# Kernel tuning notes

Hardware: AMD Instinct MI355X
Metric: run time of the kernel (lower is better)

## Reference

```python
import jax, jax.numpy as jnp
import numpy as np

NUM_EMBEDDINGS = 512
EMBEDDING_DIM = 64
COMMITMENT_COST = 0.25


def setup_inputs() -> dict:
    key = jax.random.key(0)
    k1, k2 = jax.random.split(key)
    inputs = jax.random.normal(k1, (32, EMBEDDING_DIM, 64, 64), dtype=jnp.float32)
    # nn.Embedding weight init: uniform(-1/K, 1/K)
    weight = jax.random.uniform(
        k2, (NUM_EMBEDDINGS, EMBEDDING_DIM), dtype=jnp.float32,
        minval=-1.0 / NUM_EMBEDDINGS, maxval=1.0 / NUM_EMBEDDINGS)
    return {"inputs": inputs, "weight": weight}


def reference(inputs, weight):
    # NCHW -> NHWC
    x = jnp.transpose(inputs, (0, 2, 3, 1))
    B, H, W, D = x.shape
    flat = x.reshape(-1, D)  # [N, D]
    # squared L2 distances to each code: [N, K]
    distances = (jnp.sum(flat * flat, axis=1, keepdims=True)
                 - 2.0 * flat @ weight.T
                 + jnp.sum(weight * weight, axis=1))
    idx = jnp.argmin(distances, axis=1)  # [N]
    # one-hot @ weight == gather (one-hot entries are exactly 0/1)
    quantized = jnp.take(weight, idx, axis=0).reshape(B, H, W, D)
    e_latent_loss = jnp.mean((jax.lax.stop_gradient(quantized) - x) ** 2)
    q_latent_loss = jnp.mean((quantized - jax.lax.stop_gradient(x)) ** 2)
    loss = q_latent_loss + COMMITMENT_COST * e_latent_loss
    # straight-through estimator
    quantized_st = x + jax.lax.stop_gradient(quantized - x)
    discrete_latent = idx.reshape(B, H, W)
    quantized_out = jnp.transpose(quantized_st, (0, 3, 1, 2))  # NHWC -> NCHW
    return discrete_latent, quantized_out, loss
```

## Files before the change

kernel.cpp:

```cpp
#include <hip/hip_runtime.h>

typedef unsigned long long ull;

#define NUM_K   512
#define DIM     64
#define N_ROWS  (32 * 64 * 64)
#define HW      4096
#define CHW     (64 * 4096)

#define IDX_OFF  0
#define Q_OFF    N_ROWS
#define LOSS_OFF (N_ROWS + 32 * 64 * 4096)

#define CAP     8
#define TILE_R4 128
#define NBLK4   (N_ROWS / TILE_R4)
#define NEPI    1024

#define WK1S    1.0e-4f
#define WK2S    2.0e-5f

#define WS_FRAG_LO   16384
#define WS_W2_OFF    32768
#define WS_SWMAX_OFF 33792
#define WS_LSL_BYTE  147456
#define WS_NEED      (147456 + NEPI * 8)

typedef __attribute__((ext_vector_type(8))) short bf16x8;
typedef __attribute__((ext_vector_type(4))) float f32x4;

typedef unsigned uGLB __attribute__((address_space(1)));
typedef unsigned uLDS __attribute__((address_space(3)));
#define GLD16(g, l) __builtin_amdgcn_global_load_lds((const uGLB*)(g), (uLDS*)(l), 16, 0, 0)

#define NP_SUMSQ64(SRC, DST)                                                   \
    do {                                                                       \
        float r_[8];                                                           \
        _Pragma("unroll")                                                      \
        for (int j_ = 0; j_ < 8; ++j_) r_[j_] = __fmul_rn((SRC)[j_], (SRC)[j_]); \
        _Pragma("unroll")                                                      \
        for (int i_ = 8; i_ < 64; i_ += 8) {                                   \
            _Pragma("unroll")                                                  \
            for (int j_ = 0; j_ < 8; ++j_)                                     \
                r_[j_] = __fadd_rn(r_[j_], __fmul_rn((SRC)[i_ + j_], (SRC)[i_ + j_])); \
        }                                                                      \
        (DST) = __fadd_rn(__fadd_rn(__fadd_rn(r_[0], r_[1]), __fadd_rn(r_[2], r_[3])), \
                          __fadd_rn(__fadd_rn(r_[4], r_[5]), __fadd_rn(r_[6], r_[7]))); \
    } while (0)

#define NP_SUMSQ64_G(XC, DST)                                                  \
    do {                                                                       \
        float r_[8];                                                           \
        _Pragma("unroll")                                                      \
        for (int j_ = 0; j_ < 8; ++j_) {                                       \
            float v_ = (XC)[(size_t)j_ * HW];                                  \
            r_[j_] = __fmul_rn(v_, v_);                                        \
        }                                                                      \
        _Pragma("unroll")                                                      \
        for (int i_ = 8; i_ < 64; i_ += 8) {                                   \
            _Pragma("unroll")                                                  \
            for (int j_ = 0; j_ < 8; ++j_) {                                   \
                float v_ = (XC)[(size_t)(i_ + j_) * HW];                       \
                r_[j_] = __fadd_rn(r_[j_], __fmul_rn(v_, v_));                 \
            }                                                                  \
        }                                                                      \
        (DST) = __fadd_rn(__fadd_rn(__fadd_rn(r_[0], r_[1]), __fadd_rn(r_[2], r_[3])), \
                          __fadd_rn(__fadd_rn(r_[4], r_[5]), __fadd_rn(r_[6], r_[7]))); \
    } while (0)

__device__ __forceinline__ unsigned bf16rn(float f) {
    unsigned u = __float_as_uint(f);
    return (u + 0x7fffu + ((u >> 16) & 1u)) >> 16;
}
__device__ __forceinline__ float bf2f(unsigned h) { return __uint_as_float(h << 16); }
__device__ __forceinline__ unsigned pk2(float lo, float hi) {
    return bf16rn(lo) | (bf16rn(hi) << 16);
}

__device__ __forceinline__ float evald(const float* __restrict__ xr,
                                       const float* __restrict__ wc,
                                       float A, float w2c) {
    float m = 0.0f;
    #pragma unroll
    for (int d = 0; d < DIM; ++d) m = __fmaf_rn(xr[d], wc[d], m);
    return __fadd_rn(__fsub_rn(A, __fmul_rn(2.0f, m)), w2c);
}
__device__ __forceinline__ float evald_g(const float* __restrict__ xcol,
                                         const float* __restrict__ wc,
                                         float A, float w2c) {
    float m = 0.0f;
    #pragma unroll
    for (int d = 0; d < DIM; ++d) m = __fmaf_rn(xcol[(size_t)d * HW], wc[d], m);
    return __fadd_rn(__fsub_rn(A, __fmul_rn(2.0f, m)), w2c);
}

__global__ __launch_bounds__(64) void vq_prep(const float* __restrict__ weight,
                                              unsigned* __restrict__ ws) {
    const int c = blockIdx.x * 64 + threadIdx.x;
    const float* wr = weight + c * DIM;
    float wv[DIM];
    #pragma unroll
    for (int d = 0; d < DIM; d += 4) {
        float4 t4 = *(const float4*)&wr[d];
        wv[d] = t4.x; wv[d + 1] = t4.y; wv[d + 2] = t4.z; wv[d + 3] = t4.w;
    }
    float s; NP_SUMSQ64(wv, s);
    ((float*)(ws + WS_W2_OFF))[c] = s;
    float sa = 0.0f;
    #pragma unroll
    for (int d = 0; d < DIM; ++d) sa = __fadd_rn(sa, fabsf(wv[d]));
    float sv = sa * 1.0002f + 1e-7f;

    const int tb = (c >> 4) * 512;
    const int ls = (c & 15) * 4;
    #pragma unroll
    for (int g = 0; g < 8; ++g) {
        int base = tb + (g >> 2) * 256 + (g & 3) * 64 + ls;
        unsigned hu[4], lu[4];
        #pragma unroll
        for (int p = 0; p < 4; ++p) {
            float e0 = wv[8 * g + 2 * p], e1 = wv[8 * g + 2 * p + 1];
            unsigned h0 = bf16rn(e0), h1 = bf16rn(e1);
            float r0 = __fsub_rn(e0, bf2f(h0));
            float r1 = __fsub_rn(e1, bf2f(h1));
            hu[p] = h0 | (h1 << 16);
            lu[p] = bf16rn(r0) | (bf16rn(r1) << 16);
        }
        *(uint4*)&ws[base] = make_uint4(hu[0], hu[1], hu[2], hu[3]);
        *(uint4*)&ws[WS_FRAG_LO + base] = make_uint4(lu[0], lu[1], lu[2], lu[3]);
    }
    #pragma unroll
    for (int mk = 1; mk <= 32; mk <<= 1) sv = fmaxf(sv, __shfl_xor(sv, mk));
    if (threadIdx.x == 0) ((float*)(ws + WS_SWMAX_OFF))[blockIdx.x] = sv;
}

__global__ __launch_bounds__(256, 3) void vq_mfma6(const float* __restrict__ x_in,
                                                   const float* __restrict__ weight,
                                                   const unsigned* __restrict__ frg,
                                                   const float* __restrict__ w2g,
                                                   float* __restrict__ out) {
    __shared__ __align__(16) unsigned dbuf[2][4096];
    __shared__ int   cntL[TILE_R4];
    __shared__ unsigned short listL[TILE_R4 * CAP];

    const int tid   = threadIdx.x;
    const int lane  = tid & 63;
    const int wid   = tid >> 6;
    const int wbase = wid * 32;
    const int qid   = lane >> 4;
    const int l15   = lane & 15;

    const int rowbase = blockIdx.x * TILE_R4;
    const int b       = rowbase >> 12;
    const int hw0     = rowbase & 4095;
    const float* xb   = x_in + (size_t)b * CHW + hw0;

    #pragma unroll
    for (int i = 0; i < 4; ++i) {
        int sg = wid * 4 + i;
        const unsigned* gsrc = frg + (sg < 8 ? sg * 256
                                             : WS_FRAG_LO + (sg - 8) * 256) + lane * 4;
        GLD16(gsrc, &dbuf[0][sg * 256]);
    }

    bf16x8 afh[2][2], afl[2][2];
    float mx[2] = {0.0f, 0.0f};
    #pragma unroll
    for (int rt = 0; rt < 2; ++rt) {
        const float* xp = xb + wbase + 16 * rt + l15;
        #pragma unroll
        for (int h = 0; h < 2; ++h) {
            const int kb = h * 32 + qid * 8;
            union { unsigned u[4]; bf16x8 v; } ch, cl;
            #pragma unroll
            for (int p = 0; p < 4; ++p) {
                float e0 = xp[(size_t)(kb + 2 * p) * HW];
                float e1 = xp[(size_t)(kb + 2 * p + 1) * HW];
                mx[rt] = fmaxf(mx[rt], fmaxf(fabsf(e0), fabsf(e1)));
                unsigned h0 = bf16rn(e0), h1 = bf16rn(e1);
                float r0 = __fsub_rn(e0, bf2f(h0));
                float r1 = __fsub_rn(e1, bf2f(h1));
                ch.u[p] = h0 | (h1 << 16);
                cl.u[p] = bf16rn(r0) | (bf16rn(r1) << 16);
            }
            afh[rt][h] = ch.v;
            afl[rt][h] = cl.v;
        }
    }
    #pragma unroll
    for (int rt = 0; rt < 2; ++rt) {
        mx[rt] = fmaxf(mx[rt], __shfl_xor(mx[rt], 16));
        mx[rt] = fmaxf(mx[rt], __shfl_xor(mx[rt], 32));
    }
    if (tid < TILE_R4) cntL[tid] = 0;

    const float* swp = (const float*)(frg + WS_SWMAX_OFF);
    float SWMAX = swp[0];
    #pragma unroll
    for (int i = 1; i < 8; ++i) SWMAX = fmaxf(SWMAX, swp[i]);

    float gthr[2][4], thr[2][4];
    #pragma unroll
    for (int rt = 0; rt < 2; ++rt)
        #pragma unroll
        for (int rg = 0; rg < 4; ++rg) {
            float mxr = __shfl(mx[rt], 4 * qid + rg);
            gthr[rt][rg] = __fmaf_rn(WK1S * mxr, 2.0f * SWMAX, WK2S);
            thr[rt][rg]  = 3.4e38f;
        }
    __syncthreads();

    for (int c = 0; c < 8; ++c) {
        const int par = c & 1;
        if (c < 7) {
            const int nxt = par ^ 1;
            const int c0  = (c + 1) * 2048;
            #pragma unroll
            for (int i = 0; i < 4; ++i) {
                int sg = wid * 4 + i;
                const unsigned* gsrc = frg + (sg < 8 ? c0 + sg * 256
                                                     : WS_FRAG_LO + c0 + (sg - 8) * 256) + lane * 4;
                GLD16(gsrc, &dbuf[nxt][sg * 256]);
            }
        }

        f32x4 acc[2][4] = {};
        #pragma unroll
        for (int jx = 0; jx < 4; ++jx) {
            const unsigned* bp = &dbuf[par][jx * 512 + lane * 4];
            bf16x8 bh0 = *(const bf16x8*)bp;
            bf16x8 bh1 = *(const bf16x8*)(bp + 256);
            bf16x8 bl0 = *(const bf16x8*)(bp + 2048);
            bf16x8 bl1 = *(const bf16x8*)(bp + 2304);
            #pragma unroll
            for (int rt = 0; rt < 2; ++rt) {
                acc[rt][jx] = __builtin_amdgcn_mfma_f32_16x16x32_bf16(afh[rt][0], bh0, acc[rt][jx], 0, 0, 0);
                acc[rt][jx] = __builtin_amdgcn_mfma_f32_16x16x32_bf16(afh[rt][1], bh1, acc[rt][jx], 0, 0, 0);
                acc[rt][jx] = __builtin_amdgcn_mfma_f32_16x16x32_bf16(afl[rt][0], bh0, acc[rt][jx], 0, 0, 0);
                acc[rt][jx] = __builtin_amdgcn_mfma_f32_16x16x32_bf16(afl[rt][1], bh1, acc[rt][jx], 0, 0, 0);
                acc[rt][jx] = __builtin_amdgcn_mfma_f32_16x16x32_bf16(afh[rt][0], bl0, acc[rt][jx], 0, 0, 0);
                acc[rt][jx] = __builtin_amdgcn_mfma_f32_16x16x32_bf16(afh[rt][1], bl1, acc[rt][jx], 0, 0, 0);
            }
        }

        float tl[2][4];
        #pragma unroll
        for (int rt = 0; rt < 2; ++rt)
            #pragma unroll
            for (int rg = 0; rg < 4; ++rg) tl[rt][rg] = 3.4e38f;
        #pragma unroll
        for (int jx = 0; jx < 4; ++jx) {
            int cd = c * 64 + jx * 16 + l15;
            float w2hv = 0.5f * w2g[cd];
            #pragma unroll
            for (int rt = 0; rt < 2; ++rt)
                #pragma unroll
                for (int rg = 0; rg < 4; ++rg) {
                    float t = __fsub_rn(w2hv, acc[rt][jx][rg]);
                    acc[rt][jx][rg] = t;
                    tl[rt][rg] = fminf(tl[rt][rg], t);
                }
        }
        #pragma unroll
        for (int mk = 1; mk <= 8; mk <<= 1)
            #pragma unroll
            for (int rt = 0; rt < 2; ++rt)
                #pragma unroll
                for (int rg = 0; rg < 4; ++rg)
                    tl[rt][rg] = fminf(tl[rt][rg], __shfl_xor(tl[rt][rg], mk));
        #pragma unroll
        for (int rt = 0; rt < 2; ++rt)
            #pragma unroll
            for (int rg = 0; rg < 4; ++rg)
                thr[rt][rg] = fminf(thr[rt][rg], __fadd_rn(tl[rt][rg], gthr[rt][rg]));

        #pragma unroll
        for (int rt = 0; rt < 2; ++rt)
            #pragma unroll
            for (int rg = 0; rg < 4; ++rg) {
                if (tl[rt][rg] <= thr[rt][rg]) {
                    #pragma unroll
                    for (int jx = 0; jx < 4; ++jx) {
                        if (acc[rt][jx][rg] <= thr[rt][rg]) {
                            int r  = wbase + 16 * rt + 4 * qid + rg;
                            int cd = c * 64 + jx * 16 + l15;
                            int cn = atomicAdd(&cntL[r], 1);
                            if (cn < CAP) listL[r * CAP + cn] = (unsigned short)cd;
                        }
                    }
                }
            }

        __syncthreads();
    }

    if (lane < 32) {
        const int r   = wbase + lane;
        const int cnt = cntL[r];
        if (cnt == 1) {
            out[IDX_OFF + rowbase + r] = (float)listL[r * CAP];
        } else if (cnt >= 2 && cnt <= CAP) {
            const float* xcol = xb + r;
            float A; NP_SUMSQ64_G(xcol, A);
            float bd = 3.4e38f; int bi = 1 << 30;
            for (int t2 = 0; t2 < cnt; ++t2) {
                int cd = listL[r * CAP + t2];
                float d2 = evald_g(xcol, weight + cd * DIM, A, w2g[cd]);
                if (d2 < bd || (d2 == bd && cd < bi)) { bd = d2; bi = cd; }
            }
            out[IDX_OFF + rowbase + r] = (float)bi;
        }
    }
    for (int rr = 0; rr < 32; ++rr) {
        int r   = wbase + rr;
        int cnt = cntL[r];
        if (cnt < 1 || cnt > CAP) {
            const float* xcol = xb + r;
            float A; NP_SUMSQ64_G(xcol, A);
            float bd = 3.4e38f; int bi = 1 << 30;
            #pragma unroll
            for (int t2 = 0; t2 < 8; ++t2) {
                int cd = t2 * 64 + lane;
                float d2 = evald_g(xcol, weight + cd * DIM, A, w2g[cd]);
                if (d2 < bd || (d2 == bd && cd < bi)) { bd = d2; bi = cd; }
            }
            ull key = ((ull)__float_as_uint(bd) << 32) | (unsigned)bi;
            #pragma unroll
            for (int mk = 1; mk <= 32; mk <<= 1) {
                ull o = __shfl_xor(key, mk);
                if (o < key) key = o;
            }
            if (lane == 0)
                out[IDX_OFF + rowbase + r] = (float)(int)(key & 0xffffffffu);
        }
    }
}

__global__ __launch_bounds__(256) void vq_epi(const float* __restrict__ x_in,
                                              const float* __restrict__ weight,
                                              double* __restrict__ lslots,
                                              float* __restrict__ out) {
    const int T = blockIdx.x * 256 + threadIdx.x;
    float lsum = 0.0f;
    #pragma unroll
    for (int u = 0; u < 8; ++u) {
        int f    = u * 262144 + T;
        int pos4 = f << 2;
        int b    = pos4 >> 18;
        int rem  = pos4 & (CHW - 1);
        int d    = rem >> 12;
        int hw4  = rem & (HW - 1);
        const float* xp = x_in + ((size_t)b << 18) + (d << 12) + hw4;
        float4 xv = *(const float4*)xp;
        float4 iv = *(const float4*)(out + IDX_OFF + (b << 12) + hw4);
        const float* wd = weight + d;
        float w0 = wd[((int)iv.x) << 6];
        float w1 = wd[((int)iv.y) << 6];
        float w2 = wd[((int)iv.z) << 6];
        float w3 = wd[((int)iv.w) << 6];
        float d0 = __fsub_rn(w0, xv.x);
        float d1 = __fsub_rn(w1, xv.y);
        float d2 = __fsub_rn(w2, xv.z);
        float d3 = __fsub_rn(w3, xv.w);
        float4 q = make_float4(__fadd_rn(xv.x, d0), __fadd_rn(xv.y, d1),
                               __fadd_rn(xv.z, d2), __fadd_rn(xv.w, d3));
        *(float4*)(out + Q_OFF + ((size_t)b << 18) + (d << 12) + hw4) = q;
        lsum = fmaf(d0, d0, lsum);
        lsum = fmaf(d1, d1, lsum);
        lsum = fmaf(d2, d2, lsum);
        lsum = fmaf(d3, d3, lsum);
    }
    #pragma unroll
    for (int off = 32; off > 0; off >>= 1) lsum += __shfl_down(lsum, off);
    __shared__ float ws4[4];
    if ((threadIdx.x & 63) == 0) ws4[threadIdx.x >> 6] = lsum;
    __syncthreads();
    if (threadIdx.x == 0)
        lslots[blockIdx.x] = (double)((ws4[0] + ws4[1]) + (ws4[2] + ws4[3]));
}

__global__ void vq_finalizeN(const double* __restrict__ lslots, int n,
                             float* __restrict__ out) {
    double s = 0.0;
    for (int i = threadIdx.x; i < n; i += 64) s += lslots[i];
    #pragma unroll
    for (int off = 32; off > 0; off >>= 1) s += __shfl_down(s, off);
    if (threadIdx.x == 0) {
        double m = s / 8388608.0;
        out[LOSS_OFF] = (float)(m + 0.25 * m);
    }
}

__global__ void vq_zero(double* __restrict__ loss_acc) {
    if (threadIdx.x == 0) *loss_acc = 0.0;
}

__global__ __launch_bounds__(256) void vq_fused(const float* __restrict__ x_in,
                                                const float* __restrict__ weight,
                                                double* __restrict__ loss_acc,
                                                float* __restrict__ out) {
    __shared__ float w2s[NUM_K];
    for (int k = threadIdx.x; k < NUM_K; k += 256) {
        const float* wk = weight + k * DIM;
        float s; NP_SUMSQ64(wk, s);
        w2s[k] = s;
    }
    __syncthreads();

    const int n  = blockIdx.x * 256 + threadIdx.x;
    const int b  = n >> 12;
    const int hw = n & 4095;
    const float* xp = x_in + b * CHW + hw;
    float x[DIM];
    #pragma unroll
    for (int d = 0; d < DIM; ++d) x[d] = xp[d * HW];

    float A; NP_SUMSQ64(x, A);

    float best = 3.4e38f;
    int   bi   = 0;
    for (int k = 0; k < NUM_K; k += 4) {
        const float* w0 = weight + k * DIM;
        float m0 = 0.f, m1 = 0.f, m2 = 0.f, m3 = 0.f;
        #pragma unroll
        for (int d = 0; d < DIM; ++d) {
            float xd = x[d];
            m0 = __fmaf_rn(xd, w0[d],           m0);
            m1 = __fmaf_rn(xd, w0[DIM + d],     m1);
            m2 = __fmaf_rn(xd, w0[2 * DIM + d], m2);
            m3 = __fmaf_rn(xd, w0[3 * DIM + d], m3);
        }
        float d0 = __fadd_rn(__fsub_rn(A, __fmul_rn(2.0f, m0)), w2s[k]);
        float d1 = __fadd_rn(__fsub_rn(A, __fmul_rn(2.0f, m1)), w2s[k + 1]);
        float d2 = __fadd_rn(__fsub_rn(A, __fmul_rn(2.0f, m2)), w2s[k + 2]);
        float d3 = __fadd_rn(__fsub_rn(A, __fmul_rn(2.0f, m3)), w2s[k + 3]);
        if (d0 < best) { best = d0; bi = k; }
        if (d1 < best) { best = d1; bi = k + 1; }
        if (d2 < best) { best = d2; bi = k + 2; }
        if (d3 < best) { best = d3; bi = k + 3; }
    }
    const int idx = bi;

    out[IDX_OFF + n] = (float)idx;
    const float* qrow = weight + idx * DIM;
    float* oq = out + Q_OFF + b * CHW + hw;
    float lsum = 0.0f;
    #pragma unroll
    for (int d = 0; d < DIM; ++d) {
        float xd   = xp[d * HW];
        float diff = __fsub_rn(qrow[d], xd);
        oq[d * HW] = __fadd_rn(xd, diff);
        lsum = fmaf(diff, diff, lsum);
    }
    #pragma unroll
    for (int off = 32; off > 0; off >>= 1) lsum += __shfl_down(lsum, off);
    __shared__ float wsum[4];
    if ((threadIdx.x & 63) == 0) wsum[threadIdx.x >> 6] = lsum;
    __syncthreads();
    if (threadIdx.x == 0)
        atomicAdd(loss_acc, (double)((wsum[0] + wsum[1]) + (wsum[2] + wsum[3])));
}

__global__ void vq_finalize(const double* __restrict__ loss_acc,
                            float* __restrict__ out) {
    double m = *loss_acc / 8388608.0;
    out[LOSS_OFF] = (float)(m + 0.25 * m);
}

extern "C" void kernel_launch(void* const* d_in, const int* in_sizes, int n_in,
                              void* d_out, int out_size, void* d_ws, size_t ws_size,
                              hipStream_t stream) {
    const float* x = (const float*)d_in[0];
    const float* w = (const float*)d_in[1];
    float* out = (float*)d_out;

    if (ws_size >= WS_NEED) {
        unsigned* ws32 = (unsigned*)d_ws;
        const float* w2g = (const float*)(ws32 + WS_W2_OFF);
        double* lslots = (double*)((char*)d_ws + WS_LSL_BYTE);
        vq_prep<<<8, 64, 0, stream>>>(w, ws32);
        vq_mfma6<<<NBLK4, 256, 0, stream>>>(x, w, ws32, w2g, out);
        vq_epi<<<NEPI, 256, 0, stream>>>(x, w, lslots, out);
        vq_finalizeN<<<1, 64, 0, stream>>>(lslots, NEPI, out);
    } else {
        double* loss_acc = (double*)d_ws;
        vq_zero<<<1, 64, 0, stream>>>(loss_acc);
        vq_fused<<<512, 256, 0, stream>>>(x, w, loss_acc, out);
        vq_finalize<<<1, 1, 0, stream>>>(loss_acc, out);
    }
}
```

Measured before the change: 192.0 us.

## Fuse epilogue into MFMA kernel and switch to 32x32x16 transposed MFMA tiles

The separate epilogue kernel that gathered the chosen codes, wrote the straight-through output and reduced the loss is folded into the distance kernel. The kernel keeps per-row winning indices in LDS and writes the quantized output directly, which removes a launch and a re-read of the index buffer. The distance GEMM is reoriented to 32x32x16 bf16 MFMAs with codes as the A operand and negated inputs as B. The accumulators are seeded with half the code norms, so the subtraction pass and most cross-lane min shuffles disappear. The trade-off is more work per block in the tail, and the epilogue's strided per-row column writes may coalesce less well than the old float4 epilogue.

```diff
diff --git a/kernel.cpp b/kernel.cpp
--- a/kernel.cpp
+++ b/kernel.cpp
@@ -13,21 +13,20 @@
 #define LOSS_OFF (N_ROWS + 32 * 64 * 4096)
 
 #define CAP     8
-#define TILE_R4 128
-#define NBLK4   (N_ROWS / TILE_R4)
-#define NEPI    1024
+#define TILE_R  128
+#define NBLK    (N_ROWS / TILE_R)
 
 #define WK1S    1.0e-4f
 #define WK2S    2.0e-5f
 
-#define WS_FRAG_LO   16384
 #define WS_W2_OFF    32768
+#define WS_W2H_OFF   33280
 #define WS_SWMAX_OFF 33792
 #define WS_LSL_BYTE  147456
-#define WS_NEED      (147456 + NEPI * 8)
-
-typedef __attribute__((ext_vector_type(8))) short bf16x8;
-typedef __attribute__((ext_vector_type(4))) float f32x4;
+#define WS_NEED      (147456 + NBLK * 8)
+
+typedef __attribute__((ext_vector_type(8)))  short bf16x8;
+typedef __attribute__((ext_vector_type(16))) float f32x16;
 
 typedef unsigned uGLB __attribute__((address_space(1)));
 typedef unsigned uLDS __attribute__((address_space(3)));
@@ -94,9 +93,10 @@
     return __fadd_rn(__fsub_rn(A, __fmul_rn(2.0f, m)), w2c);
 }
 
-__global__ __launch_bounds__(64) void vq_prep(const float* __restrict__ weight,
-                                              unsigned* __restrict__ ws) {
+__global__ __launch_bounds__(64) void vq_prep8(const float* __restrict__ weight,
+                                               unsigned* __restrict__ ws) {
     const int c = blockIdx.x * 64 + threadIdx.x;
+    const int T = c >> 5, m = c & 31;
     const float* wr = weight + c * DIM;
     float wv[DIM];
     #pragma unroll
@@ -105,52 +105,60 @@
         wv[d] = t4.x; wv[d + 1] = t4.y; wv[d + 2] = t4.z; wv[d + 3] = t4.w;
     }
     float s; NP_SUMSQ64(wv, s);
-    ((float*)(ws + WS_W2_OFF))[c] = s;
+    ((float*)(ws + WS_W2_OFF))[c]  = s;
+    ((float*)(ws + WS_W2H_OFF))[c] = 0.5f * s;
     float sa = 0.0f;
     #pragma unroll
     for (int d = 0; d < DIM; ++d) sa = __fadd_rn(sa, fabsf(wv[d]));
     float sv = sa * 1.0002f + 1e-7f;
 
-    const int tb = (c >> 4) * 512;
-    const int ls = (c & 15) * 4;
-    #pragma unroll
-    for (int g = 0; g < 8; ++g) {
-        int base = tb + (g >> 2) * 256 + (g & 3) * 64 + ls;
-        unsigned hu[4], lu[4];
-        #pragma unroll
-        for (int p = 0; p < 4; ++p) {
-            float e0 = wv[8 * g + 2 * p], e1 = wv[8 * g + 2 * p + 1];
-            unsigned h0 = bf16rn(e0), h1 = bf16rn(e1);
-            float r0 = __fsub_rn(e0, bf2f(h0));
-            float r1 = __fsub_rn(e1, bf2f(h1));
-            hu[p] = h0 | (h1 << 16);
-            lu[p] = bf16rn(r0) | (bf16rn(r1) << 16);
-        }
-        *(uint4*)&ws[base] = make_uint4(hu[0], hu[1], hu[2], hu[3]);
-        *(uint4*)&ws[WS_FRAG_LO + base] = make_uint4(lu[0], lu[1], lu[2], lu[3]);
+    #pragma unroll
+    for (int s4 = 0; s4 < 4; ++s4) {
+        const int gH = (T * 4 + s4) * 2, gL = gH + 1;
+        #pragma unroll
+        for (int kh = 0; kh < 2; ++kh) {
+            unsigned hu[4], lu[4];
+            #pragma unroll
+            for (int p = 0; p < 4; ++p) {
+                float e0 = wv[16 * s4 + 8 * kh + 2 * p];
+                float e1 = wv[16 * s4 + 8 * kh + 2 * p + 1];
+                unsigned h0 = bf16rn(e0), h1 = bf16rn(e1);
+                float r0 = __fsub_rn(e0, bf2f(h0));
+                float r1 = __fsub_rn(e1, bf2f(h1));
+                hu[p] = h0 | (h1 << 16);
+                lu[p] = bf16rn(r0) | (bf16rn(r1) << 16);
+            }
+            const int slot = (m + 32 * kh) * 4;
+            *(uint4*)&ws[gH * 256 + slot] = make_uint4(hu[0], hu[1], hu[2], hu[3]);
+            *(uint4*)&ws[gL * 256 + slot] = make_uint4(lu[0], lu[1], lu[2], lu[3]);
+        }
     }
     #pragma unroll
     for (int mk = 1; mk <= 32; mk <<= 1) sv = fmaxf(sv, __shfl_xor(sv, mk));
     if (threadIdx.x == 0) ((float*)(ws + WS_SWMAX_OFF))[blockIdx.x] = sv;
 }
 
-__global__ __launch_bounds__(256, 3) void vq_mfma6(const float* __restrict__ x_in,
+__global__ __launch_bounds__(256, 3) void vq_mfma8(const float* __restrict__ x_in,
                                                    const float* __restrict__ weight,
                                                    const unsigned* __restrict__ frg,
                                                    const float* __restrict__ w2g,
+                                                   const float* __restrict__ w2h,
+                                                   double* __restrict__ lslots,
                                                    float* __restrict__ out) {
     __shared__ __align__(16) unsigned dbuf[2][4096];
-    __shared__ int   cntL[TILE_R4];
-    __shared__ unsigned short listL[TILE_R4 * CAP];
+    __shared__ int   cntL[TILE_R];
+    __shared__ unsigned short listL[TILE_R * CAP];
+    __shared__ int   ilds[TILE_R];
+    __shared__ float wsum[4];
 
     const int tid   = threadIdx.x;
     const int lane  = tid & 63;
     const int wid   = tid >> 6;
     const int wbase = wid * 32;
-    const int qid   = lane >> 4;
-    const int l15   = lane & 15;
-
-    const int rowbase = blockIdx.x * TILE_R4;
+    const int n31   = lane & 31;
+    const int kh    = lane >> 5;
+
+    const int rowbase = blockIdx.x * TILE_R;
     const int b       = rowbase >> 12;
     const int hw0     = rowbase & 4095;
     const float* xb   = x_in + (size_t)b * CHW + hw0;
@@ -158,138 +166,112 @@
     #pragma unroll
     for (int i = 0; i < 4; ++i) {
         int sg = wid * 4 + i;
-        const unsigned* gsrc = frg + (sg < 8 ? sg * 256
-                                             : WS_FRAG_LO + (sg - 8) * 256) + lane * 4;
-        GLD16(gsrc, &dbuf[0][sg * 256]);
-    }
-
-    bf16x8 afh[2][2], afl[2][2];
-    float mx[2] = {0.0f, 0.0f};
-    #pragma unroll
-    for (int rt = 0; rt < 2; ++rt) {
-        const float* xp = xb + wbase + 16 * rt + l15;
-        #pragma unroll
-        for (int h = 0; h < 2; ++h) {
-            const int kb = h * 32 + qid * 8;
-            union { unsigned u[4]; bf16x8 v; } ch, cl;
-            #pragma unroll
-            for (int p = 0; p < 4; ++p) {
-                float e0 = xp[(size_t)(kb + 2 * p) * HW];
-                float e1 = xp[(size_t)(kb + 2 * p + 1) * HW];
-                mx[rt] = fmaxf(mx[rt], fmaxf(fabsf(e0), fabsf(e1)));
-                unsigned h0 = bf16rn(e0), h1 = bf16rn(e1);
-                float r0 = __fsub_rn(e0, bf2f(h0));
-                float r1 = __fsub_rn(e1, bf2f(h1));
-                ch.u[p] = h0 | (h1 << 16);
-                cl.u[p] = bf16rn(r0) | (bf16rn(r1) << 16);
-            }
-            afh[rt][h] = ch.v;
-            afl[rt][h] = cl.v;
-        }
-    }
-    #pragma unroll
-    for (int rt = 0; rt < 2; ++rt) {
-        mx[rt] = fmaxf(mx[rt], __shfl_xor(mx[rt], 16));
-        mx[rt] = fmaxf(mx[rt], __shfl_xor(mx[rt], 32));
-    }
-    if (tid < TILE_R4) cntL[tid] = 0;
+        GLD16(frg + sg * 256 + lane * 4, &dbuf[0][sg * 256]);
+    }
+
+    bf16x8 bh[4], bl[4];
+    float mx = 0.0f;
+    const float* xp = xb + wbase + n31;
+    #pragma unroll
+    for (int s = 0; s < 4; ++s) {
+        union { unsigned u[4]; bf16x8 v; } ch, cl;
+        #pragma unroll
+        for (int p = 0; p < 4; ++p) {
+            const int k0 = 16 * s + 8 * kh + 2 * p;
+            float x0 = xp[(size_t)k0 * HW];
+            float x1 = xp[(size_t)(k0 + 1) * HW];
+            mx = fmaxf(mx, fmaxf(fabsf(x0), fabsf(x1)));
+            float e0 = -x0, e1 = -x1;
+            unsigned h0 = bf16rn(e0), h1 = bf16rn(e1);
+            float r0 = __fsub_rn(e0, bf2f(h0));
+            float r1 = __fsub_rn(e1, bf2f(h1));
+            ch.u[p] = h0 | (h1 << 16);
+            cl.u[p] = bf16rn(r0) | (bf16rn(r1) << 16);
+        }
+        bh[s] = ch.v;
+        bl[s] = cl.v;
+    }
+    mx = fmaxf(mx, __shfl_xor(mx, 32));
+    if (tid < TILE_R) cntL[tid] = 0;
 
     const float* swp = (const float*)(frg + WS_SWMAX_OFF);
     float SWMAX = swp[0];
     #pragma unroll
     for (int i = 1; i < 8; ++i) SWMAX = fmaxf(SWMAX, swp[i]);
-
-    float gthr[2][4], thr[2][4];
-    #pragma unroll
-    for (int rt = 0; rt < 2; ++rt)
-        #pragma unroll
-        for (int rg = 0; rg < 4; ++rg) {
-            float mxr = __shfl(mx[rt], 4 * qid + rg);
-            gthr[rt][rg] = __fmaf_rn(WK1S * mxr, 2.0f * SWMAX, WK2S);
-            thr[rt][rg]  = 3.4e38f;
-        }
+    const float gthr = __fmaf_rn(WK1S * mx, 2.0f * SWMAX, WK2S);
+    float thr = 3.4e38f;
     __syncthreads();
 
     for (int c = 0; c < 8; ++c) {
         const int par = c & 1;
         if (c < 7) {
             const int nxt = par ^ 1;
-            const int c0  = (c + 1) * 2048;
             #pragma unroll
             for (int i = 0; i < 4; ++i) {
                 int sg = wid * 4 + i;
-                const unsigned* gsrc = frg + (sg < 8 ? c0 + sg * 256
-                                                     : WS_FRAG_LO + c0 + (sg - 8) * 256) + lane * 4;
-                GLD16(gsrc, &dbuf[nxt][sg * 256]);
-            }
-        }
-
-        f32x4 acc[2][4] = {};
-        #pragma unroll
-        for (int jx = 0; jx < 4; ++jx) {
-            const unsigned* bp = &dbuf[par][jx * 512 + lane * 4];
-            bf16x8 bh0 = *(const bf16x8*)bp;
-            bf16x8 bh1 = *(const bf16x8*)(bp + 256);
-            bf16x8 bl0 = *(const bf16x8*)(bp + 2048);
-            bf16x8 bl1 = *(const bf16x8*)(bp + 2304);
+                GLD16(frg + (c + 1) * 4096 + sg * 256 + lane * 4,
+                      &dbuf[nxt][sg * 256]);
+            }
+        }
+
+        f32x16 acc0, acc1;
+        {
+            const float* wa = w2h + (2 * c) * 32 + 4 * kh;
+            float4 a0 = *(const float4*)&wa[0];
+            float4 a1 = *(const float4*)&wa[8];
+            float4 a2 = *(const float4*)&wa[16];
+            float4 a3 = *(const float4*)&wa[24];
+            acc0[0]=a0.x; acc0[1]=a0.y; acc0[2]=a0.z; acc0[3]=a0.w;
+            acc0[4]=a1.x; acc0[5]=a1.y; acc0[6]=a1.z; acc0[7]=a1.w;
+            acc0[8]=a2.x; acc0[9]=a2.y; acc0[10]=a2.z; acc0[11]=a2.w;
+            acc0[12]=a3.x; acc0[13]=a3.y; acc0[14]=a3.z; acc0[15]=a3.w;
+            const float* wb = w2h + (2 * c + 1) * 32 + 4 * kh;
+            float4 c0 = *(const float4*)&wb[0];
+            float4 c1 = *(const float4*)&wb[8];
+            float4 c2 = *(const float4*)&wb[16];
+            float4 c3 = *(const float4*)&wb[24];
+            acc1[0]=c0.x; acc1[1]=c0.y; acc1[2]=c0.z; acc1[3]=c0.w;
+            acc1[4]=c1.x; acc1[5]=c1.y; acc1[6]=c1.z; acc1[7]=c1.w;
+            acc1[8]=c2.x; acc1[9]=c2.y; acc1[10]=c2.z; acc1[11]=c2.w;
+            acc1[12]=c3.x; acc1[13]=c3.y; acc1[14]=c3.z; acc1[15]=c3.w;
+        }
+
+        #pragma unroll
+        for (int s = 0; s < 4; ++s) {
+            bf16x8 ah0 = *(const bf16x8*)&dbuf[par][(s * 2 + 0) * 256 + lane * 4];
+            bf16x8 al0 = *(const bf16x8*)&dbuf[par][(s * 2 + 1) * 256 + lane * 4];
+            bf16x8 ah1 = *(const bf16x8*)&dbuf[par][(8 * 256) + (s * 2 + 0) * 256 + lane * 4];
+            bf16x8 al1 = *(const bf16x8*)&dbuf[par][(8 * 256) + (s * 2 + 1) * 256 + lane * 4];
+            acc0 = __builtin_amdgcn_mfma_f32_32x32x16_bf16(ah0, bh[s], acc0, 0, 0, 0);
+            acc1 = __builtin_amdgcn_mfma_f32_32x32x16_bf16(ah1, bh[s], acc1, 0, 0, 0);
+            acc0 = __builtin_amdgcn_mfma_f32_32x32x16_bf16(al0, bh[s], acc0, 0, 0, 0);
+            acc1 = __builtin_amdgcn_mfma_f32_32x32x16_bf16(al1, bh[s], acc1, 0, 0, 0);
+            acc0 = __builtin_amdgcn_mfma_f32_32x32x16_bf16(ah0, bl[s], acc0, 0, 0, 0);
+            acc1 = __builtin_amdgcn_mfma_f32_32x32x16_bf16(ah1, bl[s], acc1, 0, 0, 0);
+        }
+
+        #pragma unroll
+        for (int tl = 0; tl < 2; ++tl) {
+            float tmin = 3.4e38f;
             #pragma unroll
-            for (int rt = 0; rt < 2; ++rt) {
-                acc[rt][jx] = __builtin_amdgcn_mfma_f32_16x16x32_bf16(afh[rt][0], bh0, acc[rt][jx], 0, 0, 0);
-                acc[rt][jx] = __builtin_amdgcn_mfma_f32_16x16x32_bf16(afh[rt][1], bh1, acc[rt][jx], 0, 0, 0);
-                acc[rt][jx] = __builtin_amdgcn_mfma_f32_16x16x32_bf16(afl[rt][0], bh0, acc[rt][jx], 0, 0, 0);
-                acc[rt][jx] = __builtin_amdgcn_mfma_f32_16x16x32_bf16(afl[rt][1], bh1, acc[rt][jx], 0, 0, 0);
-                acc[rt][jx] = __builtin_amdgcn_mfma_f32_16x16x32_bf16(afh[rt][0], bl0, acc[rt][jx], 0, 0, 0);
-                acc[rt][jx] = __builtin_amdgcn_mfma_f32_16x16x32_bf16(afh[rt][1], bl1, acc[rt][jx], 0, 0, 0);
-            }
-        }
-
-        float tl[2][4];
-        #pragma unroll
-        for (int rt = 0; rt < 2; ++rt)
-            #pragma unroll
-            for (int rg = 0; rg < 4; ++rg) tl[rt][rg] = 3.4e38f;
-        #pragma unroll
-        for (int jx = 0; jx < 4; ++jx) {
-            int cd = c * 64 + jx * 16 + l15;
-            float w2hv = 0.5f * w2g[cd];
-            #pragma unroll
-            for (int rt = 0; rt < 2; ++rt)
+            for (int r = 0; r < 16; ++r)
+                tmin = fminf(tmin, (tl ? acc1[r] : acc0[r]));
+            float tlr = fminf(tmin, __shfl_xor(tmin, 32));
+            thr = fminf(thr, __fadd_rn(tlr, gthr));
+            if (tmin <= thr) {
+                const int cb = (2 * c + tl) * 32 + 4 * kh;
+                const int rr = wbase + n31;
                 #pragma unroll
-                for (int rg = 0; rg < 4; ++rg) {
-                    float t = __fsub_rn(w2hv, acc[rt][jx][rg]);
-                    acc[rt][jx][rg] = t;
-                    tl[rt][rg] = fminf(tl[rt][rg], t);
-                }
-        }
-        #pragma unroll
-        for (int mk = 1; mk <= 8; mk <<= 1)
-            #pragma unroll
-            for (int rt = 0; rt < 2; ++rt)
-                #pragma unroll
-                for (int rg = 0; rg < 4; ++rg)
-                    tl[rt][rg] = fminf(tl[rt][rg], __shfl_xor(tl[rt][rg], mk));
-        #pragma unroll
-        for (int rt = 0; rt < 2; ++rt)
-            #pragma unroll
-            for (int rg = 0; rg < 4; ++rg)
-                thr[rt][rg] = fminf(thr[rt][rg], __fadd_rn(tl[rt][rg], gthr[rt][rg]));
-
-        #pragma unroll
-        for (int rt = 0; rt < 2; ++rt)
-            #pragma unroll
-            for (int rg = 0; rg < 4; ++rg) {
-                if (tl[rt][rg] <= thr[rt][rg]) {
-                    #pragma unroll
-                    for (int jx = 0; jx < 4; ++jx) {
-                        if (acc[rt][jx][rg] <= thr[rt][rg]) {
-                            int r  = wbase + 16 * rt + 4 * qid + rg;
-                            int cd = c * 64 + jx * 16 + l15;
-                            int cn = atomicAdd(&cntL[r], 1);
-                            if (cn < CAP) listL[r * CAP + cn] = (unsigned short)cd;
-                        }
+                for (int r = 0; r < 16; ++r) {
+                    float tv = (tl ? acc1[r] : acc0[r]);
+                    if (tv <= thr) {
+                        int code = cb + (r & 3) + 8 * (r >> 2);
+                        int cn = atomicAdd(&cntL[rr], 1);
+                        if (cn < CAP) listL[rr * CAP + cn] = (unsigned short)code;
                     }
                 }
             }
+        }
 
         __syncthreads();
     }
@@ -298,7 +280,9 @@
         const int r   = wbase + lane;
         const int cnt = cntL[r];
         if (cnt == 1) {
-            out[IDX_OFF + rowbase + r] = (float)listL[r * CAP];
+            int bi = listL[r * CAP];
+            ilds[r] = bi;
+            out[IDX_OFF + rowbase + r] = (float)bi;
         } else if (cnt >= 2 && cnt <= CAP) {
             const float* xcol = xb + r;
             float A; NP_SUMSQ64_G(xcol, A);
@@ -308,6 +292,7 @@
                 float d2 = evald_g(xcol, weight + cd * DIM, A, w2g[cd]);
                 if (d2 < bd || (d2 == bd && cd < bi)) { bd = d2; bi = cd; }
             }
+            ilds[r] = bi;
             out[IDX_OFF + rowbase + r] = (float)bi;
         }
     }
@@ -330,53 +315,39 @@
                 ull o = __shfl_xor(key, mk);
                 if (o < key) key = o;
             }
-            if (lane == 0)
-                out[IDX_OFF + rowbase + r] = (float)(int)(key & 0xffffffffu);
-        }
-    }
-}
-
-__global__ __launch_bounds__(256) void vq_epi(const float* __restrict__ x_in,
-                                              const float* __restrict__ weight,
-                                              double* __restrict__ lslots,
-                                              float* __restrict__ out) {
-    const int T = blockIdx.x * 256 + threadIdx.x;
+            if (lane == 0) {
+                int bi2 = (int)(key & 0xffffffffu);
+                ilds[r] = bi2;
+                out[IDX_OFF + rowbase + r] = (float)bi2;
+            }
+        }
+    }
+    __syncthreads();
+
+    const int row = wbase + (lane & 31);
+    const int dh  = (lane >> 5) << 5;
+    const float* xcol = xb + row;
+    const float* wr2  = weight + ilds[row] * DIM + dh;
+    float* ob = out + Q_OFF + (size_t)b * CHW + hw0 + row;
     float lsum = 0.0f;
     #pragma unroll
-    for (int u = 0; u < 8; ++u) {
-        int f    = u * 262144 + T;
-        int pos4 = f << 2;
-        int b    = pos4 >> 18;
-        int rem  = pos4 & (CHW - 1);
-        int d    = rem >> 12;
-        int hw4  = rem & (HW - 1);
-        const float* xp = x_in + ((size_t)b << 18) + (d << 12) + hw4;
-        float4 xv = *(const float4*)xp;
-        float4 iv = *(const float4*)(out + IDX_OFF + (b << 12) + hw4);
-        const float* wd = weight + d;
-        float w0 = wd[((int)iv.x) << 6];
-        float w1 = wd[((int)iv.y) << 6];
-        float w2 = wd[((int)iv.z) << 6];
-        float w3 = wd[((int)iv.w) << 6];
-        float d0 = __fsub_rn(w0, xv.x);
-        float d1 = __fsub_rn(w1, xv.y);
-        float d2 = __fsub_rn(w2, xv.z);
-        float d3 = __fsub_rn(w3, xv.w);
-        float4 q = make_float4(__fadd_rn(xv.x, d0), __fadd_rn(xv.y, d1),
-                               __fadd_rn(xv.z, d2), __fadd_rn(xv.w, d3));
-        *(float4*)(out + Q_OFF + ((size_t)b << 18) + (d << 12) + hw4) = q;
-        lsum = fmaf(d0, d0, lsum);
-        lsum = fmaf(d1, d1, lsum);
-        lsum = fmaf(d2, d2, lsum);
-        lsum = fmaf(d3, d3, lsum);
+    for (int j = 0; j < 32; ++j) {
+        float xd   = xcol[(size_t)(dh + j) * HW];
+        float wq   = wr2[j];
+        float diff = __fsub_rn(wq, xd);
+        ob[(size_t)(dh + j) * HW] = __fadd_rn(xd, diff);
+        lsum = fmaf(diff, diff, lsum);
     }
     #pragma unroll
     for (int off = 32; off > 0; off >>= 1) lsum += __shfl_down(lsum, off);
-    __shared__ float ws4[4];
-    if ((threadIdx.x & 63) == 0) ws4[threadIdx.x >> 6] = lsum;
+    if (lane == 0) wsum[wid] = lsum;
     __syncthreads();
-    if (threadIdx.x == 0)
-        lslots[blockIdx.x] = (double)((ws4[0] + ws4[1]) + (ws4[2] + ws4[3]));
+    if (tid == 0) {
+        double s = 0.0;
+        #pragma unroll
+        for (int i = 0; i < 4; ++i) s += (double)wsum[i];
+        lslots[blockIdx.x] = s;
+    }
 }
 
 __global__ void vq_finalizeN(const double* __restrict__ lslots, int n,
@@ -477,11 +448,11 @@
     if (ws_size >= WS_NEED) {
         unsigned* ws32 = (unsigned*)d_ws;
         const float* w2g = (const float*)(ws32 + WS_W2_OFF);
+        const float* w2h = (const float*)(ws32 + WS_W2H_OFF);
         double* lslots = (double*)((char*)d_ws + WS_LSL_BYTE);
-        vq_prep<<<8, 64, 0, stream>>>(w, ws32);
-        vq_mfma6<<<NBLK4, 256, 0, stream>>>(x, w, ws32, w2g, out);
-        vq_epi<<<NEPI, 256, 0, stream>>>(x, w, lslots, out);
-        vq_finalizeN<<<1, 64, 0, stream>>>(lslots, NEPI, out);
+        vq_prep8<<<8, 64, 0, stream>>>(w, ws32);
+        vq_mfma8<<<NBLK, 256, 0, stream>>>(x, w, ws32, w2g, w2h, lslots, out);
+        vq_finalizeN<<<1, 64, 0, stream>>>(lslots, NBLK, out);
     } else {
         double* loss_acc = (double*)d_ws;
         vq_zero<<<1, 64, 0, stream>>>(loss_acc);
```

Measured after the change: 158.5 us. 1.21x faster.
